# Performance work log

Measured on AMD Instinct MI355X. Metric: run time of the kernel, lower is better.

The kernel has to match this reference:

```python
import jax, jax.numpy as jnp
import numpy as np

N_HEADS = 16
D_EMBED = 1024
D_HEAD = D_EMBED // N_HEADS
CAUSAL = False


def setup_inputs() -> dict:
    key = jax.random.key(0)
    k1, k2, k3, k4, k5 = jax.random.split(key, 5)
    B, S, D = 4, 2048, D_EMBED
    scale = 1.0 / np.sqrt(D)
    return {
        "x": jax.random.normal(k1, (B, S, D), dtype=jnp.float32),
        "w_in": jax.random.normal(k2, (D, 3 * D), dtype=jnp.float32) * scale,
        "b_in": jax.random.normal(k3, (3 * D,), dtype=jnp.float32) * 0.02,
        "w_out": jax.random.normal(k4, (D, D), dtype=jnp.float32) * scale,
        "b_out": jax.random.normal(k5, (D,), dtype=jnp.float32) * 0.02,
    }


def reference(x, w_in, b_in, w_out, b_out):
    B, S, D = x.shape
    qkv = jnp.einsum("bsd,de->bse", x, w_in) + b_in  # [B,S,3D]
    q, k, v = jnp.split(qkv, 3, axis=-1)
    # split heads -> [B,H,S,Dh]
    def sh(t):
        return t.reshape(B, S, N_HEADS, D_HEAD).transpose(0, 2, 1, 3)
    q, k, v = sh(q), sh(k), sh(v)
    weight = jnp.einsum("bhsd,bhtd->bhst", q, k)  # [B,H,S,S]
    if CAUSAL:
        mask = jnp.triu(jnp.ones((S, S), dtype=bool), k=1)
        weight = jnp.where(mask, -jnp.inf, weight)
    weight = weight / np.sqrt(D_HEAD)
    weight = jax.nn.softmax(weight, axis=-1)
    out = jnp.einsum("bhst,bhtd->bhsd", weight, v)
    out = out.transpose(0, 2, 1, 3).reshape(B, S, D)
    return jnp.einsum("bsd,de->bse", out, w_out) + b_out
```

## Files before the change

### kernel.cpp

```cpp
#include <hip/hip_runtime.h>
#include <hip/hip_bf16.h>

typedef unsigned short u16;
typedef __attribute__((ext_vector_type(8))) short bf16x8;
typedef __attribute__((ext_vector_type(4))) float f32x4;

#define QSCALE 0.180336880f

#define DEV static __device__ __forceinline__

DEV u16 f2bf(float f) {
  union { float f; unsigned u; } v; v.f = f;
  unsigned r = v.u + 0x7fffu + ((v.u >> 16) & 1u);
  return (u16)(r >> 16);
}

DEV unsigned pk2(float a, float b) {
  union { __hip_bfloat162 h; unsigned u; } c;
  c.h = __float22bfloat162_rn(make_float2(a, b));
  return c.u;
}

DEV void gll16(void* lds, const void* g) {
  __builtin_amdgcn_global_load_lds(
      (const __attribute__((address_space(1))) unsigned int*)g,
      (__attribute__((address_space(3))) unsigned int*)lds, 16, 0, 0);
}

__global__ __launch_bounds__(256) void cvt_f32_to_bf16(const float* __restrict__ in,
                                                       u16* __restrict__ out, int n4) {
  int i = blockIdx.x * blockDim.x + threadIdx.x;
  int stride = gridDim.x * blockDim.x;
  for (; i < n4; i += stride) {
    float4 f = ((const float4*)in)[i];
    ushort4 u;
    u.x = f2bf(f.x); u.y = f2bf(f.y); u.z = f2bf(f.z); u.w = f2bf(f.w);
    ((ushort4*)out)[i] = u;
  }
}

__global__ __launch_bounds__(256) void transpose_cvt(const float* __restrict__ W,
                                                     u16* __restrict__ Wt,
                                                     int K, int N, int sn, float sval) {
  __shared__ u16 t[64][65];
  const int k0 = blockIdx.x * 64, n0 = blockIdx.y * 64;
  const int tid = threadIdx.x;
  const int rr = tid >> 4;
  const int cc = (tid & 15) * 4;
  const float scl = (n0 < sn) ? sval : 1.0f;
#pragma unroll
  for (int i = 0; i < 4; ++i) {
    const int row = rr * 4 + i;
    float4 f = *(const float4*)&W[(size_t)(k0 + row) * N + n0 + cc];
    t[row][cc + 0] = f2bf(f.x * scl);
    t[row][cc + 1] = f2bf(f.y * scl);
    t[row][cc + 2] = f2bf(f.z * scl);
    t[row][cc + 3] = f2bf(f.w * scl);
  }
  __syncthreads();
#pragma unroll
  for (int i = 0; i < 4; ++i) {
    const int n = rr * 4 + i;
    ushort4 u;
    u.x = t[cc + 0][n]; u.y = t[cc + 1][n]; u.z = t[cc + 2][n]; u.w = t[cc + 3][n];
    *(ushort4*)&Wt[(size_t)(n0 + n) * K + k0 + cc] = u;
  }
}

__global__ __launch_bounds__(256) void transpose_v(const u16* __restrict__ qkv,
                                                   u16* __restrict__ vT) {
  __shared__ u16 t[64][72];
  const int bh = blockIdx.y;
  const int b = bh >> 4, h = bh & 15;
  const int t0 = blockIdx.x * 64;
  const int tid = threadIdx.x;
  const int row = tid >> 2;
  const int cg = (tid & 3) * 16;
  const size_t src = (size_t)b * 2048 * 3072 + (size_t)(t0 + row) * 3072 + 2048 + h * 64 + cg;
  bf16x8 v0 = *(const bf16x8*)&qkv[src];
  bf16x8 v1 = *(const bf16x8*)&qkv[src + 8];
#pragma unroll
  for (int i = 0; i < 8; ++i) { t[row][cg + i] = (u16)v0[i]; t[row][cg + 8 + i] = (u16)v1[i]; }
  __syncthreads();
  const int d = tid >> 2;
  const int tg = (tid & 3) * 16;
  bf16x8 o0, o1;
#pragma unroll
  for (int i = 0; i < 8; ++i) { o0[i] = (short)t[tg + i][d]; o1[i] = (short)t[tg + 8 + i][d]; }
  u16* dst = &vT[((size_t)bh * 64 + d) * 2048 + t0 + tg];
  *(bf16x8*)dst = o0;
  *(bf16x8*)(dst + 8) = o1;
}

template<bool OUT_BF16>
__global__ __launch_bounds__(256) void gemm_bf16(const u16* __restrict__ A,
                                                 const u16* __restrict__ Bt,
                                                 const float* __restrict__ bias,
                                                 void* __restrict__ Cout,
                                                 int M, int N, int K, int qn,
                                                 u16* __restrict__ vTout, int vn0) {
  __shared__ __align__(16) u16 As[128][64];
  __shared__ __align__(16) u16 Bs[128][64];
  const int tid = threadIdx.x;
  const int wave = tid >> 6, lane = tid & 63;
  const int g = lane >> 4, lr = lane & 15;
  const int bm = blockIdx.x * 128, bn = blockIdx.y * 128;
  const int wm = (wave >> 1) * 64, wn = (wave & 1) * 64;
  f32x4 acc[4][4] = {};
  for (int kt = 0; kt < K; kt += 64) {
    __syncthreads();
#pragma unroll
    for (int j = 0; j < 4; ++j) {
      int chunk = wave * 4 + j;
      int e = chunk * 512 + lane * 8;
      int r = e >> 6, c = e & 63;
      gll16((u16*)As + chunk * 512, &A[(size_t)(bm + r) * K + kt + c]);
      gll16((u16*)Bs + chunk * 512, &Bt[(size_t)(bn + r) * K + kt + c]);
    }
    __syncthreads();
#pragma unroll
    for (int kk = 0; kk < 64; kk += 32) {
      bf16x8 af[4], bfr[4];
#pragma unroll
      for (int m = 0; m < 4; ++m)
        af[m] = *(const bf16x8*)&As[wm + m * 16 + lr][kk + g * 8];
#pragma unroll
      for (int n = 0; n < 4; ++n)
        bfr[n] = *(const bf16x8*)&Bs[wn + n * 16 + lr][kk + g * 8];
#pragma unroll
      for (int m = 0; m < 4; ++m)
#pragma unroll
        for (int n = 0; n < 4; ++n)
          acc[m][n] = __builtin_amdgcn_mfma_f32_16x16x32_bf16(af[m], bfr[n], acc[m][n], 0, 0, 0);
    }
  }
#pragma unroll
  for (int m = 0; m < 4; ++m) {
#pragma unroll
    for (int n = 0; n < 4; ++n) {
      const int col = bn + wn + n * 16 + lr;
      float bv = bias ? bias[col] : 0.f;
      if (col < qn) bv *= QSCALE;
      if (vTout != nullptr && col >= vn0) {
        const int hc = col - vn0;
#pragma unroll
        for (int r = 0; r < 4; ++r) {
          const int row = bm + wm + m * 16 + g * 4 + r;
          const size_t idx = (((size_t)(row >> 11) * 16 + (hc >> 6)) * 64 + (hc & 63)) * 2048
                             + (row & 2047);
          vTout[idx] = f2bf(acc[m][n][r] + bv);
        }
      } else {
#pragma unroll
        for (int r = 0; r < 4; ++r) {
          const int row = bm + wm + m * 16 + g * 4 + r;
          float v = acc[m][n][r] + bv;
          if (OUT_BF16) ((u16*)Cout)[(size_t)row * N + col] = f2bf(v);
          else          ((float*)Cout)[(size_t)row * N + col] = v;
        }
      }
    }
  }
}


#define ATTN_BODY(BUF, PRE)                                                     \
  {                                                                             \
    if (PRE) {                                                                  \
      gll16((u16*)Ks[(BUF) ^ 1] + c0 * 512, gk0); gk0 += 64 * 3072;             \
      gll16((u16*)Ks[(BUF) ^ 1] + c1 * 512, gk1); gk1 += 64 * 3072;             \
      gll16((u16*)Vs[(BUF) ^ 1] + c0 * 512, gv0); gv0 += 64;                    \
      gll16((u16*)Vs[(BUF) ^ 1] + c1 * 512, gv1); gv1 += 64;                    \
    }                                                                           \
    const char* kb = (const char*)Ks[(BUF)];                                    \
    const char* vb = (const char*)Vs[(BUF)];                                    \
    f32x4 s[4] = {};                                                            \
    _Pragma("unroll")                                                           \
    for (int kk = 0; kk < 2; ++kk)                                              \
      _Pragma("unroll")                                                         \
      for (int n = 0; n < 4; ++n) {                                             \
        bf16x8 kf = *(const bf16x8*)(kb + off[kk][n]);                          \
        s[n] = __builtin_amdgcn_mfma_f32_16x16x32_bf16(kf, qf[kk], s[n], 0, 0, 0); \
      }                                                                         \
    f32x4 t01, t23;                                                             \
    _Pragma("unroll")                                                           \
    for (int i = 0; i < 4; ++i) {                                               \
      t01[i] = fmaxf(s[0][i], s[1][i]);                                         \
      t23[i] = fmaxf(s[2][i], s[3][i]);                                         \
    }                                                                           \
    float pmax = fmaxf(fmaxf(fmaxf(t01[0], t23[0]), fmaxf(t01[1], t23[1])),     \
                       fmaxf(fmaxf(t01[2], t23[2]), fmaxf(t01[3], t23[3])));    \
    if (!__all(pmax <= m + 8.f)) {                                              \
      float pm = fmaxf(pmax, __shfl_xor(pmax, 16));                             \
      pm = fmaxf(pm, __shfl_xor(pm, 32));                                       \
      float mnew = fmaxf(m, pm);                                                \
      float sc = __builtin_amdgcn_exp2f(m - mnew);                              \
      float sc0 = __shfl(sc, g * 4 + 0);                                        \
      float sc1 = __shfl(sc, g * 4 + 1);                                        \
      float sc2 = __shfl(sc, g * 4 + 2);                                        \
      float sc3 = __shfl(sc, g * 4 + 3);                                        \
      _Pragma("unroll")                                                         \
      for (int nd = 0; nd < 4; ++nd) {                                          \
        o[nd][0] *= sc0; o[nd][1] *= sc1; o[nd][2] *= sc2; o[nd][3] *= sc3;     \
      }                                                                         \
      lsum *= sc;                                                               \
      m = mnew;                                                                 \
    }                                                                           \
    float su = 0.f;                                                             \
    _Pragma("unroll")                                                           \
    for (int n = 0; n < 4; ++n) {                                               \
      float p0 = __builtin_amdgcn_exp2f(s[n][0] - m);                           \
      float p1 = __builtin_amdgcn_exp2f(s[n][1] - m);                           \
      float p2 = __builtin_amdgcn_exp2f(s[n][2] - m);                           \
      float p3 = __builtin_amdgcn_exp2f(s[n][3] - m);                           \
      uint2 w;                                                                  \
      w.x = pk2(p0, p1);                                                        \
      w.y = pk2(p2, p3);                                                        \
      *(uint2*)(pb + pwo[n]) = w;                                               \
      su += (p0 + p1) + (p2 + p3);                                              \
    }                                                                           \
    lsum += su;                                                                 \
    _Pragma("unroll")                                                           \
    for (int kk = 0; kk < 2; ++kk) {                                            \
      bf16x8 pf = *(const bf16x8*)(pb + off[kk][0]);                            \
      _Pragma("unroll")                                                         \
      for (int nd = 0; nd < 4; ++nd) {                                          \
        bf16x8 vf = *(const bf16x8*)(vb + off[kk][nd]);                         \
        o[nd] = __builtin_amdgcn_mfma_f32_16x16x32_bf16(pf, vf, o[nd], 0, 0, 0); \
      }                                                                         \
    }                                                                           \
    __syncthreads();                                                            \
  }

__global__ __launch_bounds__(256) void attn_kernel(const u16* __restrict__ qkv,
                                                   const u16* __restrict__ vT,
                                                   u16* __restrict__ out) {
  __shared__ __align__(16) u16 Ks[2][4096];
  __shared__ __align__(16) u16 Vs[2][4096];
  __shared__ __align__(16) u16 Ps[4][1024];
  const int tid = threadIdx.x;
  const int wave = tid >> 6, lane = tid & 63;
  const int g = lane >> 4, lr = lane & 15;
  const int bh = blockIdx.y;
  const int b = bh >> 4, h = bh & 15;
  const int q0 = blockIdx.x * 64;
  const size_t base = (size_t)b * 2048 * 3072;
  const u16* kg = qkv + base + 1024 + h * 64;
  const u16* vg = vT + (size_t)bh * 64 * 2048;

  const int qrow = q0 + wave * 16 + lr;
  bf16x8 qf[2];
#pragma unroll
  for (int kk = 0; kk < 2; ++kk)
    qf[kk] = *(const bf16x8*)&qkv[base + (size_t)qrow * 3072 + h * 64 + kk * 32 + g * 8];

  const int sw = (lr & 7) << 4;
  int off[2][4];
#pragma unroll
  for (int kk = 0; kk < 2; ++kk)
#pragma unroll
    for (int n = 0; n < 4; ++n)
      off[kk][n] = (n * 16 + lr) * 128 + ((kk * 64 + g * 16) ^ sw);
  int pwo[4];
#pragma unroll
  for (int n = 0; n < 4; ++n)
    pwo[n] = lr * 128 + ((n * 32 + g * 8) ^ sw);
  char* const pb = (char*)Ps[wave];

  const int c0 = wave * 2, c1 = c0 + 1;
  const int a0 = c0 * 1024 + lane * 16, a1 = c1 * 1024 + lane * 16;
  const int r0 = a0 >> 7, r1 = a1 >> 7;
  const int cb0 = (a0 & 127) ^ ((r0 & 7) << 4), cb1 = (a1 & 127) ^ ((r1 & 7) << 4);
  const u16* gk0 = kg + (size_t)r0 * 3072 + (cb0 >> 1);
  const u16* gk1 = kg + (size_t)r1 * 3072 + (cb1 >> 1);
  const u16* gv0 = vg + (size_t)r0 * 2048 + (cb0 >> 1);
  const u16* gv1 = vg + (size_t)r1 * 2048 + (cb1 >> 1);

  f32x4 o[4] = {};
  float m = -1e30f, lsum = 0.f;

  gll16((u16*)Ks[0] + c0 * 512, gk0); gk0 += 64 * 3072;
  gll16((u16*)Ks[0] + c1 * 512, gk1); gk1 += 64 * 3072;
  gll16((u16*)Vs[0] + c0 * 512, gv0); gv0 += 64;
  gll16((u16*)Vs[0] + c1 * 512, gv1); gv1 += 64;
  __syncthreads();

  for (int it2 = 0; it2 < 16; ++it2) {
    ATTN_BODY(0, 1)
    ATTN_BODY(1, it2 < 15)
  }

  float lf = lsum + __shfl_xor(lsum, 16);
  lf += __shfl_xor(lf, 32);
  float l0 = __shfl(lf, g * 4 + 0);
  float l1 = __shfl(lf, g * 4 + 1);
  float l2 = __shfl(lf, g * 4 + 2);
  float l3 = __shfl(lf, g * 4 + 3);
  const size_t orow0 = (size_t)b * 2048 + q0 + wave * 16;
#pragma unroll
  for (int nd = 0; nd < 4; ++nd) {
    const int dcol = h * 64 + nd * 16 + lr;
    out[(orow0 + g * 4 + 0) * 1024 + dcol] = f2bf(o[nd][0] / l0);
    out[(orow0 + g * 4 + 1) * 1024 + dcol] = f2bf(o[nd][1] / l1);
    out[(orow0 + g * 4 + 2) * 1024 + dcol] = f2bf(o[nd][2] / l2);
    out[(orow0 + g * 4 + 3) * 1024 + dcol] = f2bf(o[nd][3] / l3);
  }
}

extern "C" void kernel_launch(void* const* d_in, const int* in_sizes, int n_in,
                              void* d_out, int out_size, void* d_ws, size_t ws_size,
                              hipStream_t stream) {
  (void)in_sizes; (void)n_in; (void)out_size;
  const float* x     = (const float*)d_in[0];
  const float* w_in  = (const float*)d_in[1];
  const float* b_in  = (const float*)d_in[2];
  const float* w_out = (const float*)d_in[3];
  const float* b_out = (const float*)d_in[4];
  float* out = (float*)d_out;

  char* ws = (char*)d_ws;
  u16* Xbf   = (u16*)ws; ws += (size_t)8192 * 1024 * 2;
  u16* WinT  = (u16*)ws; ws += (size_t)3072 * 1024 * 2;
  u16* WoutT = (u16*)ws; ws += (size_t)1024 * 1024 * 2;
  u16* qkv   = (u16*)ws; ws += (size_t)8192 * 3072 * 2;
  u16* attno = (u16*)ws; ws += (size_t)8192 * 1024 * 2;
  u16* vTsep = (u16*)ws;

  const size_t fused_need = 92274688ull + 16777216ull;
  const bool fused = (ws_size >= fused_need);
  u16* vT = fused ? vTsep : Xbf;

  cvt_f32_to_bf16<<<2048, 256, 0, stream>>>(x, Xbf, 8192 * 1024 / 4);
  transpose_cvt<<<dim3(16, 48), 256, 0, stream>>>(w_in, WinT, 1024, 3072, 1024, QSCALE);
  transpose_cvt<<<dim3(16, 16), 256, 0, stream>>>(w_out, WoutT, 1024, 1024, 0, 1.0f);
  if (fused) {
    gemm_bf16<true ><<<dim3(64, 24), 256, 0, stream>>>(Xbf, WinT, b_in, qkv,
                                                       8192, 3072, 1024, 1024, vT, 2048);
  } else {
    gemm_bf16<true ><<<dim3(64, 24), 256, 0, stream>>>(Xbf, WinT, b_in, qkv,
                                                       8192, 3072, 1024, 1024, nullptr, 1 << 30);
    transpose_v<<<dim3(32, 64), 256, 0, stream>>>(qkv, vT);
  }
  attn_kernel<<<dim3(32, 64), 256, 0, stream>>>(qkv, vT, attno);
  gemm_bf16<false><<<dim3(64, 8), 256, 0, stream>>>(attno, WoutT, b_out, out,
                                                    8192, 1024, 1024, 0, nullptr, 1 << 30);
}
```

Baseline: 253.2 us.

## Process two 16-row query tiles per wave to reuse K/V LDS fragments

Result: no change. 254.8 us (+0.6%).

```diff
diff --git a/kernel.cpp b/kernel.cpp
--- a/kernel.cpp
+++ b/kernel.cpp
@@ -164,72 +164,87 @@
 }
 
 
-#define ATTN_BODY(BUF, PRE)                                                     \
-  {                                                                             \
-    if (PRE) {                                                                  \
-      gll16((u16*)Ks[(BUF) ^ 1] + c0 * 512, gk0); gk0 += 64 * 3072;             \
-      gll16((u16*)Ks[(BUF) ^ 1] + c1 * 512, gk1); gk1 += 64 * 3072;             \
-      gll16((u16*)Vs[(BUF) ^ 1] + c0 * 512, gv0); gv0 += 64;                    \
-      gll16((u16*)Vs[(BUF) ^ 1] + c1 * 512, gv1); gv1 += 64;                    \
-    }                                                                           \
-    const char* kb = (const char*)Ks[(BUF)];                                    \
-    const char* vb = (const char*)Vs[(BUF)];                                    \
-    f32x4 s[4] = {};                                                            \
-    _Pragma("unroll")                                                           \
-    for (int kk = 0; kk < 2; ++kk)                                              \
-      _Pragma("unroll")                                                         \
-      for (int n = 0; n < 4; ++n) {                                             \
-        bf16x8 kf = *(const bf16x8*)(kb + off[kk][n]);                          \
-        s[n] = __builtin_amdgcn_mfma_f32_16x16x32_bf16(kf, qf[kk], s[n], 0, 0, 0); \
-      }                                                                         \
-    f32x4 t01, t23;                                                             \
-    _Pragma("unroll")                                                           \
-    for (int i = 0; i < 4; ++i) {                                               \
-      t01[i] = fmaxf(s[0][i], s[1][i]);                                         \
-      t23[i] = fmaxf(s[2][i], s[3][i]);                                         \
-    }                                                                           \
-    float pmax = fmaxf(fmaxf(fmaxf(t01[0], t23[0]), fmaxf(t01[1], t23[1])),     \
-                       fmaxf(fmaxf(t01[2], t23[2]), fmaxf(t01[3], t23[3])));    \
-    if (!__all(pmax <= m + 8.f)) {                                              \
-      float pm = fmaxf(pmax, __shfl_xor(pmax, 16));                             \
-      pm = fmaxf(pm, __shfl_xor(pm, 32));                                       \
-      float mnew = fmaxf(m, pm);                                                \
-      float sc = __builtin_amdgcn_exp2f(m - mnew);                              \
-      float sc0 = __shfl(sc, g * 4 + 0);                                        \
-      float sc1 = __shfl(sc, g * 4 + 1);                                        \
-      float sc2 = __shfl(sc, g * 4 + 2);                                        \
-      float sc3 = __shfl(sc, g * 4 + 3);                                        \
-      _Pragma("unroll")                                                         \
-      for (int nd = 0; nd < 4; ++nd) {                                          \
-        o[nd][0] *= sc0; o[nd][1] *= sc1; o[nd][2] *= sc2; o[nd][3] *= sc3;     \
-      }                                                                         \
-      lsum *= sc;                                                               \
-      m = mnew;                                                                 \
-    }                                                                           \
-    float su = 0.f;                                                             \
-    _Pragma("unroll")                                                           \
-    for (int n = 0; n < 4; ++n) {                                               \
-      float p0 = __builtin_amdgcn_exp2f(s[n][0] - m);                           \
-      float p1 = __builtin_amdgcn_exp2f(s[n][1] - m);                           \
-      float p2 = __builtin_amdgcn_exp2f(s[n][2] - m);                           \
-      float p3 = __builtin_amdgcn_exp2f(s[n][3] - m);                           \
-      uint2 w;                                                                  \
-      w.x = pk2(p0, p1);                                                        \
-      w.y = pk2(p2, p3);                                                        \
-      *(uint2*)(pb + pwo[n]) = w;                                               \
-      su += (p0 + p1) + (p2 + p3);                                              \
-    }                                                                           \
-    lsum += su;                                                                 \
-    _Pragma("unroll")                                                           \
-    for (int kk = 0; kk < 2; ++kk) {                                            \
-      bf16x8 pf = *(const bf16x8*)(pb + off[kk][0]);                            \
-      _Pragma("unroll")                                                         \
-      for (int nd = 0; nd < 4; ++nd) {                                          \
-        bf16x8 vf = *(const bf16x8*)(vb + off[kk][nd]);                         \
-        o[nd] = __builtin_amdgcn_mfma_f32_16x16x32_bf16(pf, vf, o[nd], 0, 0, 0); \
-      }                                                                         \
-    }                                                                           \
-    __syncthreads();                                                            \
+DEV float rowmax(const f32x4* s) {
+  f32x4 t01, t23;
+#pragma unroll
+  for (int i = 0; i < 4; ++i) {
+    t01[i] = fmaxf(s[0][i], s[1][i]);
+    t23[i] = fmaxf(s[2][i], s[3][i]);
+  }
+  return fmaxf(fmaxf(fmaxf(t01[0], t23[0]), fmaxf(t01[1], t23[1])),
+               fmaxf(fmaxf(t01[2], t23[2]), fmaxf(t01[3], t23[3])));
+}
+
+DEV void rescale(f32x4* o, float& lsum, float& m, float pm, int g) {
+  float a = fmaxf(pm, __shfl_xor(pm, 16));
+  a = fmaxf(a, __shfl_xor(a, 32));
+  float mn = fmaxf(m, a);
+  float sc = __builtin_amdgcn_exp2f(m - mn);
+  float x0 = __shfl(sc, g * 4 + 0), x1 = __shfl(sc, g * 4 + 1);
+  float x2 = __shfl(sc, g * 4 + 2), x3 = __shfl(sc, g * 4 + 3);
+#pragma unroll
+  for (int nd = 0; nd < 4; ++nd) {
+    o[nd][0] *= x0; o[nd][1] *= x1; o[nd][2] *= x2; o[nd][3] *= x3;
+  }
+  lsum *= sc;
+  m = mn;
+}
+
+DEV float expwrite(const f32x4* s, float m, char* pbase, const int* pwo) {
+  float su = 0.f;
+#pragma unroll
+  for (int n = 0; n < 4; ++n) {
+    float p0 = __builtin_amdgcn_exp2f(s[n][0] - m);
+    float p1 = __builtin_amdgcn_exp2f(s[n][1] - m);
+    float p2 = __builtin_amdgcn_exp2f(s[n][2] - m);
+    float p3 = __builtin_amdgcn_exp2f(s[n][3] - m);
+    uint2 w;
+    w.x = pk2(p0, p1);
+    w.y = pk2(p2, p3);
+    *(uint2*)(pbase + pwo[n]) = w;
+    su += (p0 + p1) + (p2 + p3);
+  }
+  return su;
+}
+
+#define ATTN_BODY(BUF, PRE)                                                       \
+  {                                                                               \
+    if (PRE) {                                                                    \
+      gll16((u16*)Ks[(BUF) ^ 1] + c0 * 512, gk0); gk0 += 64 * 3072;               \
+      gll16((u16*)Ks[(BUF) ^ 1] + c1 * 512, gk1); gk1 += 64 * 3072;               \
+      gll16((u16*)Vs[(BUF) ^ 1] + c0 * 512, gv0); gv0 += 64;                      \
+      gll16((u16*)Vs[(BUF) ^ 1] + c1 * 512, gv1); gv1 += 64;                      \
+    }                                                                             \
+    const char* kb = (const char*)Ks[(BUF)];                                      \
+    const char* vb = (const char*)Vs[(BUF)];                                      \
+    f32x4 s0[4] = {}, s1[4] = {};                                                 \
+    _Pragma("unroll")                                                             \
+    for (int kk = 0; kk < 2; ++kk)                                                \
+      _Pragma("unroll")                                                           \
+      for (int n = 0; n < 4; ++n) {                                               \
+        bf16x8 kf = *(const bf16x8*)(kb + off[kk][n]);                            \
+        s0[n] = __builtin_amdgcn_mfma_f32_16x16x32_bf16(kf, qf0[kk], s0[n], 0, 0, 0); \
+        s1[n] = __builtin_amdgcn_mfma_f32_16x16x32_bf16(kf, qf1[kk], s1[n], 0, 0, 0); \
+      }                                                                           \
+    float pm0 = rowmax(s0), pm1 = rowmax(s1);                                     \
+    if (!__all((pm0 <= m0 + 8.f) && (pm1 <= m1 + 8.f))) {                         \
+      rescale(o0, lsum0, m0, pm0, g);                                             \
+      rescale(o1, lsum1, m1, pm1, g);                                             \
+    }                                                                             \
+    lsum0 += expwrite(s0, m0, pb, pwo);                                           \
+    lsum1 += expwrite(s1, m1, pb + 2048, pwo);                                    \
+    _Pragma("unroll")                                                             \
+    for (int kk = 0; kk < 2; ++kk) {                                              \
+      bf16x8 pf0 = *(const bf16x8*)(pb + off[kk][0]);                             \
+      bf16x8 pf1 = *(const bf16x8*)(pb + off[kk][1]);                             \
+      _Pragma("unroll")                                                           \
+      for (int nd = 0; nd < 4; ++nd) {                                            \
+        bf16x8 vf = *(const bf16x8*)(vb + off[kk][nd]);                           \
+        o0[nd] = __builtin_amdgcn_mfma_f32_16x16x32_bf16(pf0, vf, o0[nd], 0, 0, 0); \
+        o1[nd] = __builtin_amdgcn_mfma_f32_16x16x32_bf16(pf1, vf, o1[nd], 0, 0, 0); \
+      }                                                                           \
+    }                                                                             \
+    __syncthreads();                                                              \
   }
 
 __global__ __launch_bounds__(256) void attn_kernel(const u16* __restrict__ qkv,
@@ -237,22 +252,24 @@
                                                    u16* __restrict__ out) {
   __shared__ __align__(16) u16 Ks[2][4096];
   __shared__ __align__(16) u16 Vs[2][4096];
-  __shared__ __align__(16) u16 Ps[4][1024];
+  __shared__ __align__(16) u16 Ps[4][2048];
   const int tid = threadIdx.x;
   const int wave = tid >> 6, lane = tid & 63;
   const int g = lane >> 4, lr = lane & 15;
   const int bh = blockIdx.y;
   const int b = bh >> 4, h = bh & 15;
-  const int q0 = blockIdx.x * 64;
+  const int q0 = blockIdx.x * 128;
   const size_t base = (size_t)b * 2048 * 3072;
   const u16* kg = qkv + base + 1024 + h * 64;
   const u16* vg = vT + (size_t)bh * 64 * 2048;
 
-  const int qrow = q0 + wave * 16 + lr;
-  bf16x8 qf[2];
-#pragma unroll
-  for (int kk = 0; kk < 2; ++kk)
-    qf[kk] = *(const bf16x8*)&qkv[base + (size_t)qrow * 3072 + h * 64 + kk * 32 + g * 8];
+  const int qrow = q0 + wave * 32 + lr;
+  bf16x8 qf0[2], qf1[2];
+#pragma unroll
+  for (int kk = 0; kk < 2; ++kk) {
+    qf0[kk] = *(const bf16x8*)&qkv[base + (size_t)qrow * 3072 + h * 64 + kk * 32 + g * 8];
+    qf1[kk] = *(const bf16x8*)&qkv[base + (size_t)(qrow + 16) * 3072 + h * 64 + kk * 32 + g * 8];
+  }
 
   const int sw = (lr & 7) << 4;
   int off[2][4];
@@ -276,8 +293,8 @@
   const u16* gv0 = vg + (size_t)r0 * 2048 + (cb0 >> 1);
   const u16* gv1 = vg + (size_t)r1 * 2048 + (cb1 >> 1);
 
-  f32x4 o[4] = {};
-  float m = -1e30f, lsum = 0.f;
+  f32x4 o0[4] = {}, o1[4] = {};
+  float m0 = -1e30f, m1 = -1e30f, lsum0 = 0.f, lsum1 = 0.f;
 
   gll16((u16*)Ks[0] + c0 * 512, gk0); gk0 += 64 * 3072;
   gll16((u16*)Ks[0] + c1 * 512, gk1); gk1 += 64 * 3072;
@@ -290,20 +307,24 @@
     ATTN_BODY(1, it2 < 15)
   }
 
-  float lf = lsum + __shfl_xor(lsum, 16);
-  lf += __shfl_xor(lf, 32);
-  float l0 = __shfl(lf, g * 4 + 0);
-  float l1 = __shfl(lf, g * 4 + 1);
-  float l2 = __shfl(lf, g * 4 + 2);
-  float l3 = __shfl(lf, g * 4 + 3);
-  const size_t orow0 = (size_t)b * 2048 + q0 + wave * 16;
+  float lf0 = lsum0 + __shfl_xor(lsum0, 16); lf0 += __shfl_xor(lf0, 32);
+  float lf1 = lsum1 + __shfl_xor(lsum1, 16); lf1 += __shfl_xor(lf1, 32);
+  float l00 = __shfl(lf0, g * 4 + 0), l01 = __shfl(lf0, g * 4 + 1);
+  float l02 = __shfl(lf0, g * 4 + 2), l03 = __shfl(lf0, g * 4 + 3);
+  float l10 = __shfl(lf1, g * 4 + 0), l11 = __shfl(lf1, g * 4 + 1);
+  float l12 = __shfl(lf1, g * 4 + 2), l13 = __shfl(lf1, g * 4 + 3);
+  const size_t orow0 = (size_t)b * 2048 + q0 + wave * 32;
 #pragma unroll
   for (int nd = 0; nd < 4; ++nd) {
     const int dcol = h * 64 + nd * 16 + lr;
-    out[(orow0 + g * 4 + 0) * 1024 + dcol] = f2bf(o[nd][0] / l0);
-    out[(orow0 + g * 4 + 1) * 1024 + dcol] = f2bf(o[nd][1] / l1);
-    out[(orow0 + g * 4 + 2) * 1024 + dcol] = f2bf(o[nd][2] / l2);
-    out[(orow0 + g * 4 + 3) * 1024 + dcol] = f2bf(o[nd][3] / l3);
+    out[(orow0 + g * 4 + 0) * 1024 + dcol] = f2bf(o0[nd][0] / l00);
+    out[(orow0 + g * 4 + 1) * 1024 + dcol] = f2bf(o0[nd][1] / l01);
+    out[(orow0 + g * 4 + 2) * 1024 + dcol] = f2bf(o0[nd][2] / l02);
+    out[(orow0 + g * 4 + 3) * 1024 + dcol] = f2bf(o0[nd][3] / l03);
+    out[(orow0 + 16 + g * 4 + 0) * 1024 + dcol] = f2bf(o1[nd][0] / l10);
+    out[(orow0 + 16 + g * 4 + 1) * 1024 + dcol] = f2bf(o1[nd][1] / l11);
+    out[(orow0 + 16 + g * 4 + 2) * 1024 + dcol] = f2bf(o1[nd][2] / l12);
+    out[(orow0 + 16 + g * 4 + 3) * 1024 + dcol] = f2bf(o1[nd][3] / l13);
   }
 }
 
@@ -341,7 +362,7 @@
                                                        8192, 3072, 1024, 1024, nullptr, 1 << 30);
     transpose_v<<<dim3(32, 64), 256, 0, stream>>>(qkv, vT);
   }
-  attn_kernel<<<dim3(32, 64), 256, 0, stream>>>(qkv, vT, attno);
+  attn_kernel<<<dim3(16, 64), 256, 0, stream>>>(qkv, vT, attno);
   gemm_bf16<false><<<dim3(64, 8), 256, 0, stream>>>(attno, WoutT, b_out, out,
                                                     8192, 1024, 1024, 0, nullptr, 1 << 30);
 }
```
